# Kernel tuning notes

Measured on AMD Instinct MI355X. Metric: run time of the kernel, lower is better.

Reference implementation:

```python
import jax, jax.numpy as jnp
import numpy as np

HIDDEN = 1024
HEADS = 16
HEAD = HIDDEN // HEADS


def _ternary_weight(key, shape):
    g = jax.random.normal(key, shape, dtype=jnp.float32)
    return jnp.where(jnp.abs(g) < 0.6, 0.0, jnp.sign(g)).astype(jnp.float32)


def setup_inputs() -> dict:
    key = jax.random.key(0)
    ks = jax.random.split(key, 10)
    x = jax.random.normal(ks[0], (2, 2048, HIDDEN), dtype=jnp.float32)
    d = {"x": x}
    names = ["q", "k", "v", "o"]
    for i, n in enumerate(names):
        d[f"w_{n}"] = _ternary_weight(ks[1 + i], (HIDDEN, HIDDEN))
        d[f"s_{n}"] = jnp.float32(0.02)  # per-layer dequant scale
        d[f"b_{n}"] = jax.random.normal(ks[5 + i], (HIDDEN,), dtype=jnp.float32) * 0.02
    return d


def _tlin(x, w, s, b):
    # dequantized ternary linear: x @ (s * w).T + b
    return jnp.einsum("bsh,oh->bso", x, w) * s + b


def reference(x, w_q, s_q, b_q, w_k, s_k, b_k, w_v, s_v, b_v, w_o, s_o, b_o):
    B, S, H = x.shape
    def split_heads(t):
        return t.reshape(B, S, HEADS, HEAD).transpose(0, 2, 1, 3)  # [B, nH, S, hd]
    q = split_heads(_tlin(x, w_q, s_q, b_q))
    k = split_heads(_tlin(x, w_k, s_k, b_k))
    v = split_heads(_tlin(x, w_v, s_v, b_v))
    scores = jnp.einsum("bhqd,bhkd->bhqk", q, k) / jnp.sqrt(jnp.float32(HEAD))
    attn = jax.nn.softmax(scores, axis=-1)
    ctx = jnp.einsum("bhqk,bhkd->bhqd", attn, v)
    ctx = ctx.transpose(0, 2, 1, 3).reshape(B, S, H)
    return _tlin(ctx, w_o, s_o, b_o)
```

## Files before the change

### kernel.cpp

```cpp
#include <hip/hip_runtime.h>
#include <hip/hip_bf16.h>

typedef unsigned short u16;
typedef __bf16 bf16x8 __attribute__((ext_vector_type(8)));
typedef __bf16 bf16x4 __attribute__((ext_vector_type(4)));
typedef float f32x4 __attribute__((ext_vector_type(4)));
typedef unsigned short u16x8 __attribute__((ext_vector_type(8)));

__device__ inline u16 f2bf(float f) {
    union { float f; unsigned u; } v; v.f = f;
    unsigned r = v.u + 0x7fffu + ((v.u >> 16) & 1u);
    return (u16)(r >> 16);
}

__global__ void convert_kernel(const float* __restrict__ x,
                               const float* __restrict__ wq, const float* __restrict__ wk,
                               const float* __restrict__ wv, const float* __restrict__ wo,
                               u16* __restrict__ dst) {
    long g = (long)blockIdx.x * blockDim.x + threadIdx.x;
    const float* src; long base;
    const long GX = 1048576, GW = 262144;
    if (g < GX)            { src = x;  base = 0; }
    else if (g < GX + GW)  { src = wq; base = GX; }
    else if (g < GX + 2*GW){ src = wk; base = GX + GW; }
    else if (g < GX + 3*GW){ src = wv; base = GX + 2*GW; }
    else                   { src = wo; base = GX + 3*GW; }
    long rel = g - base;
    float4 v = reinterpret_cast<const float4*>(src)[rel];
    ushort4 o;
    o.x = f2bf(v.x); o.y = f2bf(v.y); o.z = f2bf(v.z); o.w = f2bf(v.w);
    reinterpret_cast<ushort4*>(dst)[g] = o;
}

__global__ void __launch_bounds__(512)
qkv_gemm(const u16* __restrict__ x_bf,
         const u16* __restrict__ wq, const u16* __restrict__ wk, const u16* __restrict__ wv,
         const float* __restrict__ sq, const float* __restrict__ sk, const float* __restrict__ sv,
         const float* __restrict__ bq, const float* __restrict__ bk, const float* __restrict__ bv,
         u16* __restrict__ q_ws, u16* __restrict__ k_ws, u16* __restrict__ v_ws) {
    __shared__ __align__(16) u16 As[2][8192];
    __shared__ __align__(16) u16 Bs[2][3 * 8192];
    const int t0 = blockIdx.x * 128, n0 = blockIdx.y * 128;

    const int tid = threadIdx.x;
    const int wid = tid >> 6, lane = tid & 63, quad = lane >> 4, ln = lane & 15;
    const int wm = wid >> 2, wn = wid & 3;

    const bool stA = (wid < 2);
    const int zz = stA ? 0 : ((wid - 2) >> 1);
    const u16* Wz = (zz == 0) ? wq : (zz == 1) ? wk : wv;
    const u16* gbase = stA ? x_bf : Wz;
    const int r0 = stA ? t0 : n0;
    const int ccb = stA ? (wid * 8) : (((wid - 2) & 1) * 8);

    const int lrow = lane >> 3;
    const int sel  = 8 * ((lane & 7) ^ lrow);

    f32x4 acc[3][4][2];
#pragma unroll
    for (int z = 0; z < 3; z++)
#pragma unroll
        for (int im = 0; im < 4; im++)
#pragma unroll
            for (int in = 0; in < 2; in++) acc[z][im][in] = (f32x4){0.f, 0.f, 0.f, 0.f};

#define QK_STAGE(buf, k0)                                                             \
    {                                                                                 \
        u16* dbase = stA ? &As[buf][0] : &Bs[buf][zz * 8192];                         \
        _Pragma("unroll")                                                             \
        for (int i = 0; i < 8; i++) {                                                 \
            int cc = ccb + i;                                                         \
            const u16* g = gbase + (long)(r0 + cc * 8 + lrow) * 1024 + (k0) + sel;    \
            __builtin_amdgcn_global_load_lds(                                         \
                (const __attribute__((address_space(1))) void*)g,                     \
                (__attribute__((address_space(3))) void*)(dbase + cc * 512), 16, 0, 0); \
        }                                                                             \
    }

    QK_STAGE(0, 0);
    __syncthreads();

    int cur = 0;
    for (int k0 = 0; k0 < 1024; k0 += 64) {
        if (k0 + 64 < 1024) QK_STAGE(cur ^ 1, k0 + 64);
        const char* Ac = (const char*)&As[cur][0];
        const char* Bc = (const char*)&Bs[cur][0];
#pragma unroll
        for (int ks = 0; ks < 2; ks++) {
            bf16x8 af[4];
#pragma unroll
            for (int im = 0; im < 4; im++) {
                int r = wm * 64 + im * 16 + ln;
                int byt = (r * 128 + ks * 64 + quad * 16) ^ ((r & 7) << 4);
                af[im] = *reinterpret_cast<const bf16x8*>(Ac + byt);
            }
            int rb = wn * 32 + ln;
#pragma unroll
            for (int z = 0; z < 3; z++) {
                bf16x8 b0, b1;
                {
                    int r = rb;
                    int byt = (r * 128 + ks * 64 + quad * 16) ^ ((r & 7) << 4);
                    b0 = *reinterpret_cast<const bf16x8*>(Bc + z * 16384 + byt);
                    r = rb + 16;
                    byt = (r * 128 + ks * 64 + quad * 16) ^ ((r & 7) << 4);
                    b1 = *reinterpret_cast<const bf16x8*>(Bc + z * 16384 + byt);
                }
                __builtin_amdgcn_s_setprio(1);
#pragma unroll
                for (int im = 0; im < 4; im++) {
                    acc[z][im][0] = __builtin_amdgcn_mfma_f32_16x16x32_bf16(af[im], b0, acc[z][im][0], 0, 0, 0);
                    acc[z][im][1] = __builtin_amdgcn_mfma_f32_16x16x32_bf16(af[im], b1, acc[z][im][1], 0, 0, 0);
                }
                __builtin_amdgcn_s_setprio(0);
            }
        }
        __syncthreads();
        cur ^= 1;
    }
#undef QK_STAGE

    const float sq_ = sq[0] * 0.125f * 1.44269504088896f;
    const float sk_ = sk[0];
    const float sv_ = sv[0];
#pragma unroll
    for (int z = 0; z < 3; z++) {
        u16* dst = (z == 0) ? q_ws : (z == 1) ? k_ws : v_ws;
        const float* bp = (z == 0) ? bq : (z == 1) ? bk : bv;
        const float s = (z == 0) ? sq_ : (z == 1) ? sk_ : sv_;
        const float be = (z == 0) ? 0.125f * 1.44269504088896f : 1.0f;
#pragma unroll
        for (int in = 0; in < 2; in++) {
            int col = n0 + wn * 32 + in * 16 + ln;
            float bias = bp[col] * be;
            int h = col >> 6, d = col & 63;
#pragma unroll
            for (int im = 0; im < 4; im++) {
                int rbase = t0 + wm * 64 + im * 16 + quad * 4;
#pragma unroll
                for (int j2 = 0; j2 < 4; j2++) {
                    int t = rbase + j2;
                    int b = t >> 11, ss = t & 2047;
                    int bh = b * 16 + h;
                    float val = acc[z][im][in][j2] * s + bias;
                    long idx = (z < 2) ? ((long)(bh * 2048 + ss) * 64 + d)
                                       : ((long)(bh * 64 + d) * 2048 + ss);
                    dst[idx] = f2bf(val);
                }
            }
        }
    }
}

#define LDP 72

__global__ void __launch_bounds__(512)
attn_kernel(const u16* __restrict__ q_ws, const u16* __restrict__ k_ws,
            const u16* __restrict__ v_ws, u16* __restrict__ ctx) {
    __shared__ __align__(16) u16 Kb[2][4096];
    __shared__ __align__(16) u16 Vb[2][4096];
    __shared__ u16 Pt[128 * LDP];

    const int tid = threadIdx.x;
    const int wid = tid >> 6, lane = tid & 63, quad = lane >> 4, ln = lane & 15;

    const int f   = blockIdx.x + 16 * blockIdx.y;
    const int xcd = f & 7, j = f >> 3;
    const int bh  = xcd * 4 + (j >> 4);
    const int q0  = (j & 15) * 128;

    const u16* qbase = q_ws + (long)bh * 2048 * 64;
    const u16* kbase = k_ws + (long)bh * 2048 * 64;
    const u16* vbase = v_ws + (long)bh * 64 * 2048;

    const int srow = wid * 8 + (lane >> 3);
    const int sel  = 8 * ((lane & 7) ^ ((lane >> 3) & 7));
    const int xr = (ln & 7) << 4;

    bf16x8 aq[2];
#pragma unroll
    for (int ks = 0; ks < 2; ks++)
        aq[ks] = *reinterpret_cast<const bf16x8*>(
            qbase + (long)(q0 + wid * 16 + ln) * 64 + ks * 32 + quad * 8);

    bf16x8 vones;
#pragma unroll
    for (int i = 0; i < 8; i++) vones[i] = (__bf16)1.0f;

    f32x4 acc_o[4];
    f32x4 acc_l = (f32x4){0.f, 0.f, 0.f, 0.f};
#pragma unroll
    for (int dt = 0; dt < 4; dt++) acc_o[dt] = (f32x4){0.f, 0.f, 0.f, 0.f};

    const u16* kp = kbase + (long)srow * 64 + sel;
    const u16* vp = vbase + (long)srow * 2048 + sel;

    __builtin_amdgcn_global_load_lds((const __attribute__((address_space(1))) void*)kp,
                                     (__attribute__((address_space(3))) void*)(&Kb[0][wid * 512]),
                                     16, 0, 0);
    __builtin_amdgcn_global_load_lds((const __attribute__((address_space(1))) void*)vp,
                                     (__attribute__((address_space(3))) void*)(&Vb[0][wid * 512]),
                                     16, 0, 0);
    kp += 4096; vp += 64;
    __syncthreads();

    int cur = 0;
    for (int kt = 0; kt < 2048; kt += 64) {
        if (kt + 64 < 2048) {
            __builtin_amdgcn_global_load_lds((const __attribute__((address_space(1))) void*)kp,
                                             (__attribute__((address_space(3))) void*)(&Kb[cur ^ 1][wid * 512]),
                                             16, 0, 0);
            __builtin_amdgcn_global_load_lds((const __attribute__((address_space(1))) void*)vp,
                                             (__attribute__((address_space(3))) void*)(&Vb[cur ^ 1][wid * 512]),
                                             16, 0, 0);
            kp += 4096; vp += 64;
        }
        const char* Kc = (const char*)(&Kb[cur][0]);
        const char* Vc = (const char*)(&Vb[cur][0]);

#pragma unroll
        for (int k8 = 0; k8 < 4; k8++) {
            bf16x8 a0 = *reinterpret_cast<const bf16x8*>(
                Kc + (k8 * 16 + ln) * 128 + ((quad * 16) ^ xr));
            bf16x8 a1 = *reinterpret_cast<const bf16x8*>(
                Kc + (k8 * 16 + ln) * 128 + ((64 + quad * 16) ^ xr));
            f32x4 t = (f32x4){0.f, 0.f, 0.f, 0.f};
            __builtin_amdgcn_s_setprio(1);
            t = __builtin_amdgcn_mfma_f32_16x16x32_bf16(a0, aq[0], t, 0, 0, 0);
            t = __builtin_amdgcn_mfma_f32_16x16x32_bf16(a1, aq[1], t, 0, 0, 0);
            __builtin_amdgcn_s_setprio(0);
            __bf16 p0 = (__bf16)__builtin_amdgcn_exp2f(t[0]);
            __bf16 p1 = (__bf16)__builtin_amdgcn_exp2f(t[1]);
            __bf16 p2 = (__bf16)__builtin_amdgcn_exp2f(t[2]);
            __bf16 p3 = (__bf16)__builtin_amdgcn_exp2f(t[3]);
            *reinterpret_cast<bf16x4*>(Pt + (wid * 16 + ln) * LDP + k8 * 16 + quad * 4)
                = (bf16x4){p0, p1, p2, p3};
        }

#pragma unroll
        for (int step = 0; step < 2; step++) {
            bf16x8 ap = *reinterpret_cast<const bf16x8*>(
                Pt + (wid * 16 + ln) * LDP + step * 32 + quad * 8);
            bf16x8 bv0 = *reinterpret_cast<const bf16x8*>(
                Vc + (0 * 16 + ln) * 128 + ((step * 64 + quad * 16) ^ xr));
            bf16x8 bv1 = *reinterpret_cast<const bf16x8*>(
                Vc + (1 * 16 + ln) * 128 + ((step * 64 + quad * 16) ^ xr));
            bf16x8 bv2 = *reinterpret_cast<const bf16x8*>(
                Vc + (2 * 16 + ln) * 128 + ((step * 64 + quad * 16) ^ xr));
            bf16x8 bv3 = *reinterpret_cast<const bf16x8*>(
                Vc + (3 * 16 + ln) * 128 + ((step * 64 + quad * 16) ^ xr));
            __builtin_amdgcn_s_setprio(1);
            acc_o[0] = __builtin_amdgcn_mfma_f32_16x16x32_bf16(ap, bv0, acc_o[0], 0, 0, 0);
            acc_o[1] = __builtin_amdgcn_mfma_f32_16x16x32_bf16(ap, bv1, acc_o[1], 0, 0, 0);
            acc_o[2] = __builtin_amdgcn_mfma_f32_16x16x32_bf16(ap, bv2, acc_o[2], 0, 0, 0);
            acc_o[3] = __builtin_amdgcn_mfma_f32_16x16x32_bf16(ap, bv3, acc_o[3], 0, 0, 0);
            acc_l    = __builtin_amdgcn_mfma_f32_16x16x32_bf16(ap, vones, acc_l, 0, 0, 0);
            __builtin_amdgcn_s_setprio(0);
        }
        __syncthreads();
        cur ^= 1;
    }

    const int b = bh >> 4, h = bh & 15;
#pragma unroll
    for (int j2 = 0; j2 < 4; j2++) {
        float rinv = 1.0f / acc_l[j2];
        int t = b * 2048 + q0 + wid * 16 + quad * 4 + j2;
#pragma unroll
        for (int dt = 0; dt < 4; dt++) {
            float val = acc_o[dt][j2] * rinv;
            ctx[(long)t * 1024 + h * 64 + dt * 16 + ln] = f2bf(val);
        }
    }
}

__global__ void __launch_bounds__(512)
o_gemm(const u16* __restrict__ ctx, const u16* __restrict__ wo,
       const float* __restrict__ so, const float* __restrict__ bo,
       float* __restrict__ out) {
    __shared__ __align__(16) u16 As[2][128 * 64];
    __shared__ __align__(16) u16 Bs[2][128 * 64];
    const int tid = threadIdx.x;
    const int wid = tid >> 6, lane = tid & 63, quad = lane >> 4, ln = lane & 15;
    const int wm = wid >> 2, wn = wid & 3;
    const int t0 = blockIdx.x * 128, n0 = blockIdx.y * 128;

    const bool stA = (wid < 4);
    const u16* gbase = stA ? ctx : wo;
    const int r0 = stA ? t0 : n0;
    const int cbase = (wid & 3) * 4;

    f32x4 acc[4][2];
#pragma unroll
    for (int im = 0; im < 4; im++)
#pragma unroll
        for (int in = 0; in < 2; in++) acc[im][in] = (f32x4){0.f, 0.f, 0.f, 0.f};

    const int sb   = cbase * 1024 + lane * 16;
    const int srow = sb >> 7;
    const int scb  = (sb & 127) ^ ((srow & 7) << 4);

#define O_STAGE(buf, k0)                                                              \
    {                                                                                 \
        const u16* g = gbase + (long)(r0 + srow) * 1024 + (k0) + (scb >> 1);          \
        u16* d = (stA ? &As[buf][0] : &Bs[buf][0]) + cbase * 512;                     \
        _Pragma("unroll")                                                             \
        for (int i = 0; i < 4; i++) {                                                 \
            __builtin_amdgcn_global_load_lds(                                         \
                (const __attribute__((address_space(1))) void*)(g + (long)i * 8 * 1024), \
                (__attribute__((address_space(3))) void*)(d + i * 512), 16, 0, 0);    \
        }                                                                             \
    }

    O_STAGE(0, 0);
    __syncthreads();

    int cur = 0;
    for (int k0 = 0; k0 < 1024; k0 += 64) {
        if (k0 + 64 < 1024) O_STAGE(cur ^ 1, k0 + 64);
        const char* Ac = (const char*)&As[cur][0];
        const char* Bc = (const char*)&Bs[cur][0];
#pragma unroll
        for (int ks = 0; ks < 2; ks++) {
            bf16x8 af[4], bfr[2];
#pragma unroll
            for (int im = 0; im < 4; im++) {
                int r = wm * 64 + im * 16 + ln;
                int byt = (r * 128 + ks * 64 + quad * 16) ^ ((r & 7) << 4);
                af[im] = *reinterpret_cast<const bf16x8*>(Ac + byt);
            }
#pragma unroll
            for (int in = 0; in < 2; in++) {
                int r = wn * 32 + in * 16 + ln;
                int byt = (r * 128 + ks * 64 + quad * 16) ^ ((r & 7) << 4);
                bfr[in] = *reinterpret_cast<const bf16x8*>(Bc + byt);
            }
#pragma unroll
            for (int im = 0; im < 4; im++)
#pragma unroll
                for (int in = 0; in < 2; in++)
                    acc[im][in] = __builtin_amdgcn_mfma_f32_16x16x32_bf16(af[im], bfr[in], acc[im][in], 0, 0, 0);
        }
        __syncthreads();
        cur ^= 1;
    }
#undef O_STAGE

    const float s = so[0];
#pragma unroll
    for (int in = 0; in < 2; in++) {
        int col = n0 + wn * 32 + in * 16 + ln;
        float bias = bo[col];
#pragma unroll
        for (int im = 0; im < 4; im++) {
            int rbase = t0 + wm * 64 + im * 16 + quad * 4;
#pragma unroll
            for (int j2 = 0; j2 < 4; j2++)
                out[(long)(rbase + j2) * 1024 + col] = acc[im][in][j2] * s + bias;
        }
    }
}

extern "C" void kernel_launch(void* const* d_in, const int* in_sizes, int n_in,
                              void* d_out, int out_size, void* d_ws, size_t ws_size,
                              hipStream_t stream) {
    const float* x   = (const float*)d_in[0];
    const float* w_q = (const float*)d_in[1];
    const float* s_q = (const float*)d_in[2];
    const float* b_q = (const float*)d_in[3];
    const float* w_k = (const float*)d_in[4];
    const float* s_k = (const float*)d_in[5];
    const float* b_k = (const float*)d_in[6];
    const float* w_v = (const float*)d_in[7];
    const float* s_v = (const float*)d_in[8];
    const float* b_v = (const float*)d_in[9];
    const float* w_o = (const float*)d_in[10];
    const float* s_o = (const float*)d_in[11];
    const float* b_o = (const float*)d_in[12];

    if (ws_size < (size_t)50331648) return;

    u16* ws     = (u16*)d_ws;
    u16* x_bf   = ws;
    u16* wq_bf  = x_bf  + 4194304;
    u16* wk_bf  = wq_bf + 1048576;
    u16* wv_bf  = wk_bf + 1048576;
    u16* wo_bf  = wv_bf + 1048576;
    u16* q_ws   = wo_bf + 1048576;
    u16* k_ws   = q_ws  + 4194304;
    u16* v_ws   = k_ws  + 4194304;
    u16* ctx_ws = v_ws  + 4194304;

    convert_kernel<<<dim3(8192), dim3(256), 0, stream>>>(x, w_q, w_k, w_v, w_o, ws);
    qkv_gemm<<<dim3(32, 8), dim3(512), 0, stream>>>(x_bf, wq_bf, wk_bf, wv_bf,
                                                    s_q, s_k, s_v, b_q, b_k, b_v,
                                                    q_ws, k_ws, v_ws);
    attn_kernel<<<dim3(16, 32), dim3(512), 0, stream>>>(q_ws, k_ws, v_ws, ctx_ws);
    o_gemm<<<dim3(32, 8), dim3(512), 0, stream>>>(ctx_ws, wo_bf, s_o, b_o, (float*)d_out);
}
```

Before: 185.5 us.

## Fuse bf16 conversion into QKV GEMM via cooperative grid sync

Merges the fp32-to-bf16 conversion kernel and the QKV GEMM into one cooperative kernel. The 256 blocks first convert x and all four weights with a grid-stride loop, then wait at a grid-wide barrier before running the GEMM. The goal is to remove one kernel launch and its gap. It falls back to the two separate kernels if the cooperative launch fails. The risks are that the grid sync has its own cost and the conversion now runs on only 256 blocks of 512 threads. The cooperative launch also needs every block to be resident at once, which the large LDS use per block may prevent.

```diff
diff --git a/kernel.cpp b/kernel.cpp
--- a/kernel.cpp
+++ b/kernel.cpp
@@ -1,5 +1,7 @@
 #include <hip/hip_runtime.h>
 #include <hip/hip_bf16.h>
+#include <hip/hip_cooperative_groups.h>
+namespace cg = cooperative_groups;
 
 typedef unsigned short u16;
 typedef __bf16 bf16x8 __attribute__((ext_vector_type(8)));
@@ -32,16 +34,15 @@
     reinterpret_cast<ushort4*>(dst)[g] = o;
 }
 
-__global__ void __launch_bounds__(512)
-qkv_gemm(const u16* __restrict__ x_bf,
-         const u16* __restrict__ wq, const u16* __restrict__ wk, const u16* __restrict__ wv,
-         const float* __restrict__ sq, const float* __restrict__ sk, const float* __restrict__ sv,
-         const float* __restrict__ bq, const float* __restrict__ bk, const float* __restrict__ bv,
-         u16* __restrict__ q_ws, u16* __restrict__ k_ws, u16* __restrict__ v_ws) {
-    __shared__ __align__(16) u16 As[2][8192];
-    __shared__ __align__(16) u16 Bs[2][3 * 8192];
+__device__ __forceinline__ void qkv_compute(
+    const u16* __restrict__ x_bf,
+    const u16* __restrict__ wq, const u16* __restrict__ wk, const u16* __restrict__ wv,
+    const float* __restrict__ sq, const float* __restrict__ sk, const float* __restrict__ sv,
+    const float* __restrict__ bq, const float* __restrict__ bk, const float* __restrict__ bv,
+    u16* __restrict__ q_ws, u16* __restrict__ k_ws, u16* __restrict__ v_ws,
+    u16* As, u16* Bs)
+{
     const int t0 = blockIdx.x * 128, n0 = blockIdx.y * 128;
-
     const int tid = threadIdx.x;
     const int wid = tid >> 6, lane = tid & 63, quad = lane >> 4, ln = lane & 15;
     const int wm = wid >> 2, wn = wid & 3;
@@ -66,7 +67,7 @@
 
 #define QK_STAGE(buf, k0)                                                             \
     {                                                                                 \
-        u16* dbase = stA ? &As[buf][0] : &Bs[buf][zz * 8192];                         \
+        u16* dbase = stA ? (As + (buf) * 8192) : (Bs + (buf) * 24576 + zz * 8192);    \
         _Pragma("unroll")                                                             \
         for (int i = 0; i < 8; i++) {                                                 \
             int cc = ccb + i;                                                         \
@@ -83,8 +84,8 @@
     int cur = 0;
     for (int k0 = 0; k0 < 1024; k0 += 64) {
         if (k0 + 64 < 1024) QK_STAGE(cur ^ 1, k0 + 64);
-        const char* Ac = (const char*)&As[cur][0];
-        const char* Bc = (const char*)&Bs[cur][0];
+        const char* Ac = (const char*)(As + cur * 8192);
+        const char* Bc = (const char*)(Bs + cur * 24576);
 #pragma unroll
         for (int ks = 0; ks < 2; ks++) {
             bf16x8 af[4];
@@ -150,6 +151,55 @@
             }
         }
     }
+}
+
+__global__ void __launch_bounds__(512)
+qkv_fused(const float* __restrict__ xf,
+          const float* __restrict__ wqf, const float* __restrict__ wkf,
+          const float* __restrict__ wvf, const float* __restrict__ wof,
+          const float* __restrict__ sq, const float* __restrict__ sk, const float* __restrict__ sv,
+          const float* __restrict__ bq, const float* __restrict__ bk, const float* __restrict__ bv,
+          u16* __restrict__ ws, u16* __restrict__ q_ws, u16* __restrict__ k_ws,
+          u16* __restrict__ v_ws) {
+    __shared__ __align__(16) u16 As[2 * 8192];
+    __shared__ __align__(16) u16 Bs[2 * 24576];
+
+    {
+        long g0 = (long)(blockIdx.x + 32 * blockIdx.y) * 512 + threadIdx.x;
+#pragma unroll 1
+        for (long g = g0; g < 2097152; g += 131072) {
+            const float* src; long base;
+            if (g < 1048576)      { src = xf;  base = 0; }
+            else if (g < 1310720) { src = wqf; base = 1048576; }
+            else if (g < 1572864) { src = wkf; base = 1310720; }
+            else if (g < 1835008) { src = wvf; base = 1572864; }
+            else                  { src = wof; base = 1835008; }
+            float4 v = reinterpret_cast<const float4*>(src)[g - base];
+            ushort4 o;
+            o.x = f2bf(v.x); o.y = f2bf(v.y); o.z = f2bf(v.z); o.w = f2bf(v.w);
+            reinterpret_cast<ushort4*>(ws)[g] = o;
+        }
+    }
+    __threadfence();
+    cg::this_grid().sync();
+
+    const u16* x_bf  = ws;
+    const u16* wq_bf = ws + 4194304;
+    const u16* wk_bf = wq_bf + 1048576;
+    const u16* wv_bf = wk_bf + 1048576;
+    qkv_compute(x_bf, wq_bf, wk_bf, wv_bf, sq, sk, sv, bq, bk, bv,
+                q_ws, k_ws, v_ws, As, Bs);
+}
+
+__global__ void __launch_bounds__(512)
+qkv_gemm(const u16* __restrict__ x_bf,
+         const u16* __restrict__ wq, const u16* __restrict__ wk, const u16* __restrict__ wv,
+         const float* __restrict__ sq, const float* __restrict__ sk, const float* __restrict__ sv,
+         const float* __restrict__ bq, const float* __restrict__ bk, const float* __restrict__ bv,
+         u16* __restrict__ q_ws, u16* __restrict__ k_ws, u16* __restrict__ v_ws) {
+    __shared__ __align__(16) u16 As[2 * 8192];
+    __shared__ __align__(16) u16 Bs[2 * 24576];
+    qkv_compute(x_bf, wq, wk, wv, sq, sk, sv, bq, bk, bv, q_ws, k_ws, v_ws, As, Bs);
 }
 
 #define LDP 72
@@ -391,10 +441,19 @@
     u16* v_ws   = k_ws  + 4194304;
     u16* ctx_ws = v_ws  + 4194304;
 
-    convert_kernel<<<dim3(8192), dim3(256), 0, stream>>>(x, w_q, w_k, w_v, w_o, ws);
-    qkv_gemm<<<dim3(32, 8), dim3(512), 0, stream>>>(x_bf, wq_bf, wk_bf, wv_bf,
-                                                    s_q, s_k, s_v, b_q, b_k, b_v,
-                                                    q_ws, k_ws, v_ws);
+    void* cargs[] = {(void*)&x, (void*)&w_q, (void*)&w_k, (void*)&w_v, (void*)&w_o,
+                     (void*)&s_q, (void*)&s_k, (void*)&s_v,
+                     (void*)&b_q, (void*)&b_k, (void*)&b_v,
+                     (void*)&ws, (void*)&q_ws, (void*)&k_ws, (void*)&v_ws};
+    hipError_t cerr = hipLaunchCooperativeKernel((const void*)qkv_fused,
+                                                 dim3(32, 8), dim3(512),
+                                                 cargs, 0, stream);
+    if (cerr != hipSuccess) {
+        convert_kernel<<<dim3(8192), dim3(256), 0, stream>>>(x, w_q, w_k, w_v, w_o, ws);
+        qkv_gemm<<<dim3(32, 8), dim3(512), 0, stream>>>(x_bf, wq_bf, wk_bf, wv_bf,
+                                                        s_q, s_k, s_v, b_q, b_k, b_v,
+                                                        q_ws, k_ws, v_ws);
+    }
     attn_kernel<<<dim3(16, 32), dim3(512), 0, stream>>>(q_ws, k_ws, v_ws, ctx_ws);
     o_gemm<<<dim3(32, 8), dim3(512), 0, stream>>>(ctx_ws, wo_bf, s_o, b_o, (float*)d_out);
 }
```

New measurement: 280.4 us. 51.2% more time.
